# Optimization experiments

Measured on AMD Instinct MI355X. Metric: run time of the kernel, lower is better.

Reference implementation:

```python
import jax, jax.numpy as jnp
import numpy as np
from jax import lax

EPS = 1e-5
GROUPS = 8
TDVD_RANGE = 10
SCALE = 1.0
SCALE_FACTOR = 0.5


def setup_inputs() -> dict:
    key = jax.random.key(0)
    k1, k2 = jax.random.split(key)
    x = jax.random.normal(k1, (2, 16, 64, 128, 128), dtype=jnp.float32)
    gn_weight = jnp.ones((16,), dtype=jnp.float32)
    gn_bias = jnp.zeros((16,), dtype=jnp.float32)
    threshold = jnp.ones((1,), dtype=jnp.float32)  # torch fills with 1.0
    conv_weight = jax.random.normal(k2, (16, 16, 3, 3, 3), dtype=jnp.float32) * 0.05
    return {"x": x, "gn_weight": gn_weight, "gn_bias": gn_bias,
            "threshold": threshold, "conv_weight": conv_weight}


def _group_norm(x, w, b):
    B, C, D, H, W = x.shape
    xr = x.reshape(B, GROUPS, C // GROUPS, D, H, W)
    mean = xr.mean(axis=(2, 3, 4, 5), keepdims=True)
    var = xr.var(axis=(2, 3, 4, 5), keepdims=True)
    xn = ((xr - mean) * lax.rsqrt(var + EPS)).reshape(B, C, D, H, W)
    return xn * w.reshape(1, C, 1, 1, 1) + b.reshape(1, C, 1, 1, 1)


def _tdvd_histogram(x):
    # reverseint(x * scale * scale_factor) counted into 21 bins [-10..10], as %.
    y = x * (SCALE * SCALE_FACTOR)
    v = jnp.ceil(y * (y >= 0)) + jnp.floor(y * (y <= 0))
    idx = (v + TDVD_RANGE).astype(jnp.int32)
    valid = (idx >= 0) & (idx <= 2 * TDVD_RANGE)
    hist = jnp.zeros((2 * TDVD_RANGE + 1,), jnp.float32).at[
        jnp.clip(idx, 0, 2 * TDVD_RANGE)].add(jnp.where(valid, 1.0, 0.0))
    return hist / x.size * 100.0


def _threshold_func(x, threshold):
    thr = (threshold[0] + 0.0) / SCALE  # zero_point=0, scale=1.0
    t = jnp.transpose(x, (2, 0, 1, 3, 4))  # [D,B,C,H,W]
    front, back = t[:-1], t[1:]
    d = (back - front) / thr
    d = jnp.where(jnp.abs(d) > 1.0, d, 0.0)  # Hardshrink(1.0)
    d = d * lax.stop_gradient(thr)           # .item() detaches in torch
    out = jnp.concatenate([t[:1], front + d], axis=0)
    return jnp.transpose(out, (1, 2, 0, 3, 4))


def reference(x, gn_weight, gn_bias, threshold, conv_weight):
    x = jax.nn.relu(_group_norm(x, gn_weight, gn_bias))
    hist = _tdvd_histogram(x)
    x = _threshold_func(x, threshold)
    out = lax.conv_general_dilated(
        x, conv_weight, window_strides=(1, 1, 1),
        padding=((1, 1), (1, 1), (1, 1)),
        dimension_numbers=("NCDHW", "OIDHW", "NCDHW"))
    return out, hist
```

## Files before the change

### kernel.cpp

```cpp
#include <hip/hip_runtime.h>

typedef __attribute__((ext_vector_type(8))) short short8;
typedef __attribute__((ext_vector_type(4))) float f32x4;

#define GROUP_ELEMS 2097152
#define NBLK 64

__device__ inline short f2bf(float f) {
  unsigned u = __builtin_bit_cast(unsigned, f);
  unsigned r = (u + 0x7FFFu + ((u >> 16) & 1u)) >> 16;
  return (short)r;
}

__device__ inline void gload_lds16(const void* g, void* l) {
  __builtin_amdgcn_global_load_lds(
      (const __attribute__((address_space(1))) unsigned int*)g,
      (__attribute__((address_space(3))) unsigned int*)l, 16, 0, 0);
}

__global__ __launch_bounds__(256) void k1_partials(const float* __restrict__ x,
                                                   float2* __restrict__ partials) {
  int group = blockIdx.x >> 6;
  int blk = blockIdx.x & 63;
  const float4* p = (const float4*)(x + (size_t)group * GROUP_ELEMS + (size_t)blk * 32768);
  float sum = 0.f, sq = 0.f;
  for (int i = threadIdx.x; i < 8192; i += 256) {
    float4 v = p[i];
    sum += v.x + v.y + v.z + v.w;
    sq  += v.x*v.x + v.y*v.y + v.z*v.z + v.w*v.w;
  }
  for (int off = 32; off; off >>= 1) {
    sum += __shfl_down(sum, off, 64);
    sq  += __shfl_down(sq,  off, 64);
  }
  __shared__ float2 sw[4];
  int lane = threadIdx.x & 63, wid = threadIdx.x >> 6;
  if (lane == 0) sw[wid] = make_float2(sum, sq);
  __syncthreads();
  if (threadIdx.x == 0) {
    float s = 0.f, q = 0.f;
    for (int j = 0; j < 4; ++j) { s += sw[j].x; q += sw[j].y; }
    partials[blockIdx.x] = make_float2(s, q);
  }
}

__global__ void k2_prep(const float2* __restrict__ partials, const float* __restrict__ wgt,
                        float2* __restrict__ stats, int* __restrict__ hist,
                        unsigned short* __restrict__ fbw2, unsigned int* __restrict__ dummy) {
  int t = threadIdx.x;
  if (t < 16) {
    float s = 0.f, q = 0.f;
    for (int j = 0; j < NBLK; ++j) { float2 p = partials[t * NBLK + j]; s += p.x; q += p.y; }
    float mean = s / (float)GROUP_ELEMS;
    float var  = q / (float)GROUP_ELEMS - mean * mean;
    stats[t] = make_float2(mean, rsqrtf(var + 1e-5f));
  }
  if (t < 21) hist[t] = 0;
  if (t < 960) {
    int f = t >> 6, lane = t & 63;
    int kd = f / 5, c = f - kd * 5;
    int m = lane & 15, g = lane >> 4;
    int icb = (g & 1) * 8, g2 = g >> 1;
    int tap = 2 * c + g2;
    short8 v;
    #pragma unroll
    for (int j = 0; j < 8; ++j)
      v[j] = (tap <= 8) ? f2bf(wgt[m * 432 + (icb + j) * 27 + kd * 9 + tap]) : (short)0;
    *(short8*)(fbw2 + t * 8) = v;
  }
  if (t >= 960 && t < 976) dummy[t - 960] = 0;
}

__global__ __launch_bounds__(256) void k3_norm_thresh_hist(
    const float* __restrict__ x, const float* __restrict__ gw, const float* __restrict__ gb,
    const float* __restrict__ thrp, const float2* __restrict__ stats,
    unsigned short* __restrict__ z, int* __restrict__ hist) {
  __shared__ int sh[21];
  int t = threadIdx.x;
  if (t < 21) sh[t] = 0;
  __syncthreads();
  int hwl = t & 31, cp = t >> 5;
  int b = blockIdx.x >> 9;
  int hw = (blockIdx.x & 511) * 32 + hwl;
  int c0 = cp * 2, c1 = c0 + 1;
  float2 st = stats[b * 8 + cp];
  float A0 = gw[c0] * st.y, B0 = gb[c0] - st.x * A0;
  float A1 = gw[c1] * st.y, B1 = gb[c1] - st.x * A1;
  float thr = thrp[0];
  const float* px0 = x + (size_t)(b * 16 + c0) * 1048576 + hw;
  const float* px1 = x + (size_t)(b * 16 + c1) * 1048576 + hw;
  unsigned* pz = (unsigned*)(z + ((size_t)b * 64 * 16384 + hw) * 16 + c0);
  int c10 = 0, c11 = 0, c12 = 0;
  float xv0 = px0[0], xv1 = px1[0];
  float xm0 = px0[16384], xm1 = px1[16384];
  float yp0 = 0.f, yp1 = 0.f;
  for (int d = 0; d < 64; ++d) {
    float n0 = 0.f, n1 = 0.f;
    if (d < 62) { n0 = px0[(d + 2) * 16384]; n1 = px1[(d + 2) * 16384]; }
    float y0 = fmaxf(fmaf(xv0, A0, B0), 0.f);
    float y1 = fmaxf(fmaf(xv1, A1, B1), 0.f);
    float v0 = ceilf(0.5f * y0);
    if (v0 == 0.f) c10++; else if (v0 == 1.f) c11++; else if (v0 == 2.f) c12++;
    else if (v0 <= 10.f) atomicAdd(&sh[(int)v0 + 10], 1);
    float v1 = ceilf(0.5f * y1);
    if (v1 == 0.f) c10++; else if (v1 == 1.f) c11++; else if (v1 == 2.f) c12++;
    else if (v1 <= 10.f) atomicAdd(&sh[(int)v1 + 10], 1);
    float z0, z1;
    if (d == 0) { z0 = y0; z1 = y1; }
    else {
      z0 = (fabsf(y0 - yp0) > thr) ? y0 : yp0;
      z1 = (fabsf(y1 - yp1) > thr) ? y1 : yp1;
    }
    unsigned u = (unsigned)(unsigned short)f2bf(z0) | ((unsigned)(unsigned short)f2bf(z1) << 16);
    pz[d * 131072] = u;
    yp0 = y0; yp1 = y1;
    xv0 = xm0; xv1 = xm1;
    xm0 = n0; xm1 = n1;
  }
  atomicAdd(&sh[10], c10);
  atomicAdd(&sh[11], c11);
  atomicAdd(&sh[12], c12);
  __syncthreads();
  if (t < 21) atomicAdd(&hist[t], sh[t]);
}

#define DT 8
#define PLANE 5440
__global__ __launch_bounds__(512, 4) void k4_conv(const unsigned short* __restrict__ z,
                                                  const unsigned short* __restrict__ fbw2,
                                                  const char* __restrict__ dummyc,
                                                  const int* __restrict__ hist,
                                                  float* __restrict__ out) {
  __shared__ unsigned short lz[2 * PLANE];
  const int t = threadIdx.x;
  if (blockIdx.x == 0 && blockIdx.y == 0 && blockIdx.z == 0 && t < 21)
    out[33554432u + t] = (float)hist[t] * (100.0f / 33554432.0f);
  const int lane = t & 63, wid = t >> 6;
  const int b = blockIdx.z;
  const int d0 = blockIdx.y * DT;
  const int h0 = (blockIdx.x >> 2) * 8, w0 = (blockIdx.x & 3) * 32;
  const int m = lane & 15, g = lane >> 4;
  const int icb = (g & 1) * 8, g2 = g >> 1;

  short8 fb2[15];
  #pragma unroll
  for (int f = 0; f < 15; ++f)
    fb2[f] = *(const short8*)(fbw2 + (f * 64 + lane) * 8);

  int tco[5];
  #pragma unroll
  for (int c = 0; c < 5; ++c) {
    int tap = 2 * c + g2; if (tap > 8) tap = 8;
    tco[c] = ((tap / 3) * 34 + (tap % 3)) * 16;
  }

  const char* zbc = (const char*)(z + (size_t)b * 16777216);

  const int cbA = wid * 64;
  const int cbB = (wid == 0) ? 512 : (wid == 1) ? 576 : 616;
  const bool hasB = (wid < 3);
  long long hobA, hobB; bool hvA, hvB;
  {
    int gi, r, rem, s, ig, hg, wg;
    gi = cbA + lane; r = gi / 68; rem = gi - r * 68; s = rem >> 1; ig = rem & 1;
    hg = h0 - 1 + r; wg = w0 - 1 + s;
    hvA = ((unsigned)hg < 128u) && ((unsigned)wg < 128u);
    hobA = ((long long)(hg * 128 + wg) * 16 + ig * 8) * 2;
    gi = cbB + lane; r = gi / 68; rem = gi - r * 68; s = rem >> 1; ig = rem & 1;
    hg = h0 - 1 + r; wg = w0 - 1 + s;
    hvB = ((unsigned)hg < 128u) && ((unsigned)wg < 128u);
    hobB = ((long long)(hg * 128 + wg) * 16 + ig * 8) * 2;
  }

  const f32x4 fzero = {0.f, 0.f, 0.f, 0.f};
  f32x4 A0[2], A1[2], A2[2];
  #pragma unroll
  for (int q = 0; q < 2; ++q) { A0[q] = fzero; A1[q] = fzero; A2[q] = fzero; }

  {
    const int dg = d0 - 1;
    const long long dgo = (long long)dg * 524288;
    const bool pd = (unsigned)dg < 64u;
    gload_lds16((pd && hvA) ? zbc + dgo + hobA : dummyc, &lz[cbA * 8]);
    if (hasB)
      gload_lds16((pd && hvB) ? zbc + dgo + hobB : dummyc, &lz[cbB * 8]);
  }
  __syncthreads();

#define BODY(PH, AS, AM, AN, DOJ2, DOJ1, DOJ0, DOLOAD, DOSTORE)                         \
  {                                                                                     \
    const int ph_ = (PH);                                                               \
    if (DOLOAD) {                                                                       \
      const int dg = d0 + ph_;                                                          \
      const long long dgo = (long long)dg * 524288;                                     \
      const bool pd = (unsigned)dg < 64u;                                               \
      const unsigned sl = ((unsigned)(ph_ + 1) & 1u) * PLANE;                           \
      gload_lds16((pd && hvA) ? zbc + dgo + hobA : dummyc, &lz[sl + cbA * 8]);          \
      if (hasB)                                                                         \
        gload_lds16((pd && hvB) ? zbc + dgo + hobB : dummyc, &lz[sl + cbB * 8]);        \
    }                                                                                   \
    const unsigned su = ((unsigned)ph_ & 1u) * PLANE;                                   \
    __builtin_amdgcn_s_setprio(1);                                                      \
    _Pragma("unroll")                                                                   \
    for (int q = 0; q < 2; ++q) {                                                       \
      const int hl = wid, wt = q;                                                       \
      const int qb = (hl * 34 + wt * 16 + m) * 16 + icb + (int)su;                      \
      _Pragma("unroll")                                                                 \
      for (int c = 0; c < 5; ++c) {                                                     \
        short8 a = *(const short8*)(&lz[qb + tco[c]]);                                  \
        if (DOJ2) AN[q] = __builtin_amdgcn_mfma_f32_16x16x32_bf16(a, fb2[c], AN[q], 0, 0, 0);      \
        if (DOJ1) AM[q] = __builtin_amdgcn_mfma_f32_16x16x32_bf16(a, fb2[5 + c], AM[q], 0, 0, 0);  \
        if (DOJ0) AS[q] = __builtin_amdgcn_mfma_f32_16x16x32_bf16(a, fb2[10 + c], AS[q], 0, 0, 0); \
      }                                                                                 \
    }                                                                                   \
    __builtin_amdgcn_s_setprio(0);                                                      \
    if (DOSTORE) {                                                                      \
      const int dd = d0 + ph_ - 2;                                                      \
      _Pragma("unroll")                                                                 \
      for (int q = 0; q < 2; ++q) {                                                     \
        const int hl = wid, wt = q;                                                     \
        float* op = out + (((size_t)(b * 16 + m) * 64 + dd) * 128 + (h0 + hl)) * 128    \
                    + w0 + wt * 16 + g * 4;                                             \
        *(float4*)op = make_float4(AS[q][0], AS[q][1], AS[q][2], AS[q][3]);             \
        AS[q] = fzero;                                                                  \
      }                                                                                 \
    }                                                                                   \
    __syncthreads();                                                                    \
  }

  BODY(0, A1, A2, A0, 1, 0, 0, 1, 0)
  BODY(1, A2, A0, A1, 1, 1, 0, 1, 0)
  BODY(2, A0, A1, A2, 1, 1, 1, 1, 1)
  #pragma unroll 1
  for (int pp = 3; pp <= 6; pp += 3) {
    BODY(pp,     A1, A2, A0, 1, 1, 1, 1, 1)
    BODY(pp + 1, A2, A0, A1, 1, 1, 1, 1, 1)
    BODY(pp + 2, A0, A1, A2, 1, 1, 1, 1, 1)
  }
  BODY(9, A1, A2, A0, 0, 0, 1, 0, 1)
#undef BODY
}

extern "C" void kernel_launch(void* const* d_in, const int* in_sizes, int n_in,
                              void* d_out, int out_size, void* d_ws, size_t ws_size,
                              hipStream_t stream) {
  (void)in_sizes; (void)n_in; (void)out_size; (void)ws_size;
  const float* x   = (const float*)d_in[0];
  const float* gw  = (const float*)d_in[1];
  const float* gb  = (const float*)d_in[2];
  const float* thr = (const float*)d_in[3];
  const float* cw  = (const float*)d_in[4];
  float* out = (float*)d_out;

  char* ws = (char*)d_ws;
  unsigned short* z = (unsigned short*)ws;
  float2* partials  = (float2*)(ws + (size_t)67108864);
  float2* stats     = (float2*)(ws + (size_t)67108864 + 8192);
  int*    hist      = (int*)  (ws + (size_t)67108864 + 8192 + 128);
  unsigned int* dummy = (unsigned int*)(ws + (size_t)67108864 + 8448);
  unsigned short* fbw2 = (unsigned short*)(ws + (size_t)67108864 + 16384);

  k1_partials<<<1024, 256, 0, stream>>>(x, partials);
  k2_prep<<<1, 1024, 0, stream>>>(partials, cw, stats, hist, fbw2, dummy);
  k3_norm_thresh_hist<<<1024, 256, 0, stream>>>(x, gw, gb, thr, stats, z, hist);
  k4_conv<<<dim3(64, 8, 2), 512, 0, stream>>>(z, fbw2, (const char*)dummy, hist, out);
}
```

Before: 133.6 us.

## Fold prep kernel into stats and norm kernels, stage z stores through LDS

Removes the single-block k2_prep launch. Weight packing and histogram zeroing move into an extra block of k1, and each k3 block now reduces the group partials itself to get its scale and shift. The k3 output of packed bf16 pairs is also transposed through a double-buffered LDS tile, so each block's global stores become one contiguous 1 KB write per depth slice instead of 4-byte writes strided by 32 bytes. In exchange, k3 gains a __syncthreads per depth iteration and every block repeats the small partials reduction.

```diff
diff --git a/kernel.cpp b/kernel.cpp
--- a/kernel.cpp
+++ b/kernel.cpp
@@ -19,7 +19,33 @@
 }
 
 __global__ __launch_bounds__(256) void k1_partials(const float* __restrict__ x,
-                                                   float2* __restrict__ partials) {
+                                                   float2* __restrict__ partials,
+                                                   const float* __restrict__ wgt,
+                                                   unsigned short* __restrict__ fbw2,
+                                                   int* __restrict__ hist,
+                                                   unsigned int* __restrict__ dummy) {
+  if (blockIdx.x == 1024) {
+    int t0 = threadIdx.x;
+    if (t0 < 21) hist[t0] = 0;
+    #pragma unroll
+    for (int it = 0; it < 4; ++it) {
+      int t = t0 + it * 256;
+      if (t < 960) {
+        int f = t >> 6, lane = t & 63;
+        int kd = f / 5, c = f - kd * 5;
+        int m = lane & 15, g = lane >> 4;
+        int icb = (g & 1) * 8, g2 = g >> 1;
+        int tap = 2 * c + g2;
+        short8 v;
+        #pragma unroll
+        for (int j = 0; j < 8; ++j)
+          v[j] = (tap <= 8) ? f2bf(wgt[m * 432 + (icb + j) * 27 + kd * 9 + tap]) : (short)0;
+        *(short8*)(fbw2 + t * 8) = v;
+      }
+      if (t >= 960 && t < 976) dummy[t - 960] = 0;
+    }
+    return;
+  }
   int group = blockIdx.x >> 6;
   int blk = blockIdx.x & 63;
   const float4* p = (const float4*)(x + (size_t)group * GROUP_ELEMS + (size_t)blk * 32768);
@@ -44,52 +70,52 @@
   }
 }
 
-__global__ void k2_prep(const float2* __restrict__ partials, const float* __restrict__ wgt,
-                        float2* __restrict__ stats, int* __restrict__ hist,
-                        unsigned short* __restrict__ fbw2, unsigned int* __restrict__ dummy) {
+__global__ __launch_bounds__(256) void k3_norm_thresh_hist(
+    const float* __restrict__ x, const float* __restrict__ gw, const float* __restrict__ gb,
+    const float* __restrict__ thrp, const float2* __restrict__ partials,
+    unsigned short* __restrict__ z, int* __restrict__ hist) {
+  __shared__ int sh[21];
+  __shared__ float4 stf[8];
+  __shared__ float red[64], redq[64];
+  __shared__ unsigned sd[2][256];
   int t = threadIdx.x;
-  if (t < 16) {
+  if (t < 21) sh[t] = 0;
+  int b = blockIdx.x >> 9;
+  if (t < 64) {
+    int gloc = t >> 3, j8 = t & 7;
+    const float2* pp = partials + (b * 8 + gloc) * NBLK + j8 * 8;
     float s = 0.f, q = 0.f;
-    for (int j = 0; j < NBLK; ++j) { float2 p = partials[t * NBLK + j]; s += p.x; q += p.y; }
+    #pragma unroll
+    for (int k = 0; k < 8; ++k) { float2 pv = pp[k]; s += pv.x; q += pv.y; }
+    red[t] = s; redq[t] = q;
+  }
+  __syncthreads();
+  if (t < 8) {
+    float s = 0.f, q = 0.f;
+    #pragma unroll
+    for (int k = 0; k < 8; ++k) { s += red[t * 8 + k]; q += redq[t * 8 + k]; }
     float mean = s / (float)GROUP_ELEMS;
     float var  = q / (float)GROUP_ELEMS - mean * mean;
-    stats[t] = make_float2(mean, rsqrtf(var + 1e-5f));
-  }
-  if (t < 21) hist[t] = 0;
-  if (t < 960) {
-    int f = t >> 6, lane = t & 63;
-    int kd = f / 5, c = f - kd * 5;
-    int m = lane & 15, g = lane >> 4;
-    int icb = (g & 1) * 8, g2 = g >> 1;
-    int tap = 2 * c + g2;
-    short8 v;
-    #pragma unroll
-    for (int j = 0; j < 8; ++j)
-      v[j] = (tap <= 8) ? f2bf(wgt[m * 432 + (icb + j) * 27 + kd * 9 + tap]) : (short)0;
-    *(short8*)(fbw2 + t * 8) = v;
-  }
-  if (t >= 960 && t < 976) dummy[t - 960] = 0;
-}
-
-__global__ __launch_bounds__(256) void k3_norm_thresh_hist(
-    const float* __restrict__ x, const float* __restrict__ gw, const float* __restrict__ gb,
-    const float* __restrict__ thrp, const float2* __restrict__ stats,
-    unsigned short* __restrict__ z, int* __restrict__ hist) {
-  __shared__ int sh[21];
-  int t = threadIdx.x;
-  if (t < 21) sh[t] = 0;
+    float rs = rsqrtf(var + 1e-5f);
+    int c0 = t * 2;
+    float A0 = gw[c0] * rs,     B0 = gb[c0] - mean * A0;
+    float A1 = gw[c0 + 1] * rs, B1 = gb[c0 + 1] - mean * A1;
+    stf[t] = make_float4(A0, B0, A1, B1);
+  }
   __syncthreads();
   int hwl = t & 31, cp = t >> 5;
-  int b = blockIdx.x >> 9;
-  int hw = (blockIdx.x & 511) * 32 + hwl;
+  int hw0 = (blockIdx.x & 511) * 32;
+  int hw = hw0 + hwl;
+  float4 st = stf[cp];
+  float A0 = st.x, B0 = st.y, A1 = st.z, B1 = st.w;
+  float thr = thrp[0];
   int c0 = cp * 2, c1 = c0 + 1;
-  float2 st = stats[b * 8 + cp];
-  float A0 = gw[c0] * st.y, B0 = gb[c0] - st.x * A0;
-  float A1 = gw[c1] * st.y, B1 = gb[c1] - st.x * A1;
-  float thr = thrp[0];
   const float* px0 = x + (size_t)(b * 16 + c0) * 1048576 + hw;
   const float* px1 = x + (size_t)(b * 16 + c1) * 1048576 + hw;
-  unsigned* pz = (unsigned*)(z + ((size_t)b * 64 * 16384 + hw) * 16 + c0);
+  unsigned* zout = (unsigned*)z;
+  const unsigned zbase = (unsigned)(b * 1048576 + hw0) * 8;
+  const int wi = (cp << 5) | ((hwl + 4 * cp) & 31);
+  const int ri = ((t & 7) << 5) | (((t >> 3) + 4 * (t & 7)) & 31);
   int c10 = 0, c11 = 0, c12 = 0;
   float xv0 = px0[0], xv1 = px1[0];
   float xm0 = px0[16384], xm1 = px1[16384];
@@ -112,7 +138,9 @@
       z1 = (fabsf(y1 - yp1) > thr) ? y1 : yp1;
     }
     unsigned u = (unsigned)(unsigned short)f2bf(z0) | ((unsigned)(unsigned short)f2bf(z1) << 16);
-    pz[d * 131072] = u;
+    sd[d & 1][wi] = u;
+    __syncthreads();
+    zout[zbase + d * 131072 + t] = sd[d & 1][ri];
     yp0 = y0; yp1 = y1;
     xv0 = xm0; xv1 = xm1;
     xm0 = n0; xm1 = n1;
@@ -255,13 +283,11 @@
   char* ws = (char*)d_ws;
   unsigned short* z = (unsigned short*)ws;
   float2* partials  = (float2*)(ws + (size_t)67108864);
-  float2* stats     = (float2*)(ws + (size_t)67108864 + 8192);
   int*    hist      = (int*)  (ws + (size_t)67108864 + 8192 + 128);
   unsigned int* dummy = (unsigned int*)(ws + (size_t)67108864 + 8448);
   unsigned short* fbw2 = (unsigned short*)(ws + (size_t)67108864 + 16384);
 
-  k1_partials<<<1024, 256, 0, stream>>>(x, partials);
-  k2_prep<<<1, 1024, 0, stream>>>(partials, cw, stats, hist, fbw2, dummy);
-  k3_norm_thresh_hist<<<1024, 256, 0, stream>>>(x, gw, gb, thr, stats, z, hist);
+  k1_partials<<<1025, 256, 0, stream>>>(x, partials, cw, fbw2, hist, dummy);
+  k3_norm_thresh_hist<<<1024, 256, 0, stream>>>(x, gw, gb, thr, partials, z, hist);
   k4_conv<<<dim3(64, 8, 2), 512, 0, stream>>>(z, fbw2, (const char*)dummy, hist, out);
 }
```

After: 122.5 us. -8.3%, faster.
